# Kernel optimization log

Measured on AMD Instinct MI355X. Metric: run time of the kernel, lower is better.

The kernel has to match this reference:

```python
import jax, jax.numpy as jnp
import numpy as np

B, L, C, H, F = 1, 256, 256, 8, 512
D = C // H
SCALE = D ** -0.5
EPS = 1e-5


def _ln(x, g, b):
    m = jnp.mean(x, axis=-1, keepdims=True)
    v = jnp.mean((x - m) ** 2, axis=-1, keepdims=True)
    return (x - m) * jax.lax.rsqrt(v + EPS) * g + b


def setup_inputs() -> dict:
    key = jax.random.key(0)
    ks = jax.random.split(key, 16)
    w = lambda k, shp: jax.random.normal(k, shp, dtype=jnp.float32) * 0.02
    return {
        "pair_repr": jax.random.normal(ks[0], (B, L, L, C), dtype=jnp.float32),
        "pair_bias": jax.random.normal(ks[1], (B, H, L, L), dtype=jnp.float32),
        "Wq": w(ks[2], (C, C)), "bq": jnp.zeros((C,), jnp.float32),
        "Wk": w(ks[3], (C, C)), "bk": jnp.zeros((C,), jnp.float32),
        "Wv": w(ks[4], (C, C)), "bv": jnp.zeros((C,), jnp.float32),
        "Wo": w(ks[5], (C, C)), "bo": jnp.zeros((C,), jnp.float32),
        "W1": w(ks[6], (F, C)), "b1": jnp.zeros((F,), jnp.float32),
        "W2": w(ks[7], (C, F)), "b2": jnp.zeros((C,), jnp.float32),
        "g1": jnp.ones((C,), jnp.float32), "be1": jnp.zeros((C,), jnp.float32),
        "g2": jnp.ones((C,), jnp.float32), "be2": jnp.zeros((C,), jnp.float32),
        "mask": jnp.ones((B, L, L), dtype=jnp.int32),
    }


def reference(pair_repr, pair_bias, Wq, bq, Wk, bk, Wv, bv, Wo, bo,
              W1, b1, W2, b2, g1, be1, g2, be2, mask):
    x = _ln(pair_repr, g1, be1)
    # projections, split heads: [B, Li, Lj, H, D]
    q = (x @ Wq.T + bq).reshape(B, L, L, H, D)
    k = (x @ Wk.T + bk).reshape(B, L, L, H, D)
    v = (x @ Wv.T + bv).reshape(B, L, L, H, D)
    # attention per column j over rows: scores[b,j,h,i,i2]
    scores = jnp.einsum('bijhd,bkjhd->bjhik', q, k) * SCALE
    scores = scores + pair_bias[:, None]           # broadcast over j
    scores = jnp.where(mask[:, None, None, :, :] == 0, -jnp.inf, scores)
    probs = jax.nn.softmax(scores, axis=-1)
    attn = jnp.einsum('bjhik,bkjhd->bijhd', probs, v).reshape(B, L, L, C)
    attn = attn @ Wo.T + bo
    pr = pair_repr + attn                          # dropout is identity in eval
    y = _ln(pr, g2, be2)
    ff = jnp.maximum(y @ W1.T + b1, 0.0) @ W2.T + b2
    return pr + ff
```

## Files before the change

### kernel.cpp

```cpp
#include <hip/hip_runtime.h>

#define L_ 256
#define C_ 256
#define H_ 8
#define D_ 32
#define F_ 512
#define M_ (L_*L_)
#define SCALE2_ 0.2550348564624926f
#define LOG2E_  1.4426950408889634f

typedef __attribute__((ext_vector_type(8))) short v8s;
typedef __attribute__((ext_vector_type(4))) float v4f;
typedef __attribute__((ext_vector_type(16))) float v16f;
#define Z16 (v16f){0,0,0,0,0,0,0,0,0,0,0,0,0,0,0,0}

__device__ __forceinline__ ushort f2bf(float f) {
  union { float f; unsigned u; } v; v.f = f;
  unsigned r = v.u + 0x7FFFu + ((v.u >> 16) & 1u);
  return (ushort)(r >> 16);
}

__device__ __forceinline__ float bf2f(ushort u) {
  union { unsigned u; float f; } v; v.u = (unsigned)u << 16;
  return v.f;
}

__device__ __forceinline__ uint cvtpk(float lo, float hi) {
  uint r;
  asm("v_cvt_pk_bf16_f32 %0, %1, %2" : "=v"(r) : "v"(lo), "v"(hi));
  return r;
}

__device__ __forceinline__ void gload16(const void* g, void* l) {
  __builtin_amdgcn_global_load_lds(
      (const __attribute__((address_space(1))) void*)g,
      (__attribute__((address_space(3))) void*)l, 16, 0, 0);
}

__device__ __forceinline__ void pl32swap(uint &a, uint &b) {
  asm volatile("v_permlane32_swap_b32 %0, %1" : "+v"(a), "+v"(b));
}

__global__ __launch_bounds__(256) void prep_k(
    const float* __restrict__ Wq, const float* __restrict__ Wk,
    const float* __restrict__ Wv, const float* __restrict__ Wo,
    const float* __restrict__ W1, const float* __restrict__ W2,
    const float* __restrict__ bq, const float* __restrict__ bk,
    const float* __restrict__ bv,
    const float* __restrict__ bias, const int* __restrict__ mask,
    ushort* __restrict__ Wqkvb, ushort* __restrict__ Wob,
    ushort* __restrict__ W1b, ushort* __restrict__ W2b,
    float* __restrict__ bqkv, float* __restrict__ bM4) {
  int idx = blockIdx.x * 256 + threadIdx.x;
  if (idx < 49152) {
    int e = idx * 4; int n = e >> 8; int k = e & 255;
    const float* src = n < 256 ? &Wq[n*256 + k]
                     : n < 512 ? &Wk[(n-256)*256 + k]
                               : &Wv[(n-512)*256 + k];
    float4 f = *(const float4*)src;
    ushort4 o = { f2bf(f.x), f2bf(f.y), f2bf(f.z), f2bf(f.w) };
    *(ushort4*)&Wqkvb[e] = o;
  } else if (idx < 65536) {
    int e = (idx - 49152) * 4;
    float4 f = *(const float4*)&Wo[e];
    ushort4 o = { f2bf(f.x), f2bf(f.y), f2bf(f.z), f2bf(f.w) };
    *(ushort4*)&Wob[e] = o;
  } else if (idx < 98304) {
    int e = (idx - 65536) * 4;
    float4 f = *(const float4*)&W1[e];
    ushort4 o = { f2bf(f.x), f2bf(f.y), f2bf(f.z), f2bf(f.w) };
    *(ushort4*)&W1b[e] = o;
  } else if (idx < 131072) {
    int e = (idx - 98304) * 4;
    float4 f = *(const float4*)&W2[e];
    ushort4 o = { f2bf(f.x), f2bf(f.y), f2bf(f.z), f2bf(f.w) };
    *(ushort4*)&W2b[e] = o;
  } else if (idx < 262144) {
    int eb = idx - 131072;
    int q32 = eb & 31, r4 = (eb >> 5) & 3, h5 = (eb >> 7) & 1;
    int c = (eb >> 8) & 7, qb = (eb >> 11) & 7, h = eb >> 14;
    int q = qb*32 + q32;
    int keyb = 32*c + 8*r4 + 4*h5;
    float4 b4 = *(const float4*)&bias[((size_t)(h*256 + q))*256 + keyb];
    int4   m4 = *(const int4*)&mask[(size_t)q*256 + keyb];
    float4 o;
    o.x = m4.x ? b4.x * LOG2E_ - 8.0f : -1e30f;
    o.y = m4.y ? b4.y * LOG2E_ - 8.0f : -1e30f;
    o.z = m4.z ? b4.z * LOG2E_ - 8.0f : -1e30f;
    o.w = m4.w ? b4.w * LOG2E_ - 8.0f : -1e30f;
    *(float4*)&bM4[(size_t)eb*4] = o;
  } else if (idx < 262336) {
    int e = (idx - 262144) * 4;
    const float* src = e < 256 ? &bq[e] : e < 512 ? &bk[e-256] : &bv[e-512];
    *(float4*)&bqkv[e] = *(const float4*)src;
  }
}

template<bool TR>
__global__ __launch_bounds__(256) void ln_k(const float* __restrict__ in,
    const float* __restrict__ g, const float* __restrict__ b,
    ushort* __restrict__ out) {
  int wid = threadIdx.x >> 6, lane = threadIdx.x & 63;
  size_t row = (size_t)blockIdx.x * 4 + wid;
  const float* x = in + row * C_;
  float4 v = *(const float4*)&x[lane*4];
  float s  = v.x + v.y + v.z + v.w;
  float s2 = v.x*v.x + v.y*v.y + v.z*v.z + v.w*v.w;
  #pragma unroll
  for (int off = 1; off < 64; off <<= 1) {
    s  += __shfl_xor(s,  off);
    s2 += __shfl_xor(s2, off);
  }
  float mean = s * (1.0f/C_);
  float var  = s2 * (1.0f/C_) - mean*mean;
  float inv  = rsqrtf(var + 1e-5f);
  float4 gg = *(const float4*)&g[lane*4];
  float4 bb = *(const float4*)&b[lane*4];
  ushort4 o;
  o.x = f2bf((v.x-mean)*inv*gg.x + bb.x);
  o.y = f2bf((v.y-mean)*inv*gg.y + bb.y);
  o.z = f2bf((v.z-mean)*inv*gg.z + bb.z);
  o.w = f2bf((v.w-mean)*inv*gg.w + bb.w);
  size_t orow = TR ? ((row & 255) * 256 + (row >> 8)) : row;
  *(ushort4*)&out[orow*C_ + lane*4] = o;
}

template<bool OUTBF16, bool RELU, bool ADD, bool ADDB, bool QKV>
__global__ __launch_bounds__(256) void gemm5(
    const ushort* __restrict__ A, const ushort* __restrict__ W,
    const float* __restrict__ bias, const void* Rp,
    void* Optr, int N, int K, int lda, int ldo, int nby) {
  __shared__ __align__(16) ushort LDSb[2][128][64];
  constexpr bool LDST = QKV || (OUTBF16 && !ADD && !ADDB);
  int f = blockIdx.x;
  int sw = (f & 7) * (gridDim.x >> 3) + (f >> 3);
  const int bm = (sw / nby) * 128;
  const int bn = (sw % nby) * 128;
  const int t  = threadIdx.x;
  const int lane = t & 63, w = t >> 6;
  const int wm = (w >> 1) * 64, wn = (w & 1) * 64;
  const int lg = lane >> 4, lc = lane & 15;
  const int srow0 = t >> 3;
  const int scc   = t & 7;

  v4f acc[4][4];
  #pragma unroll
  for (int i = 0; i < 4; ++i)
    #pragma unroll
    for (int jj = 0; jj < 4; ++jj) acc[i][jj] = (v4f){0.f,0.f,0.f,0.f};

  for (int k0 = 0; k0 < K; k0 += 64) {
    #pragma unroll
    for (int s = 0; s < 4; ++s) {
      int row = s*32 + srow0;
      int gc  = (scc ^ (row & 7)) * 8;
      gload16(&A[(size_t)(bm + row)*lda + k0 + gc], (char*)LDSb + s*4096 + t*16);
      gload16(&W[(size_t)(bn + row)*K  + k0 + gc], (char*)LDSb + 16384 + s*4096 + t*16);
    }
    __syncthreads();
    #pragma unroll
    for (int kh = 0; kh < 2; ++kh) {
      v8s af[4], bf_[4];
      #pragma unroll
      for (int mi = 0; mi < 4; ++mi) {
        int row = wm + mi*16 + lc;
        int cd  = ((kh*4 + lg) ^ (row & 7)) * 16;
        af[mi] = *(const v8s*)((const char*)LDSb + row*128 + cd);
      }
      #pragma unroll
      for (int ni = 0; ni < 4; ++ni) {
        int row = wn + ni*16 + lc;
        int cd  = ((kh*4 + lg) ^ (row & 7)) * 16;
        bf_[ni] = *(const v8s*)((const char*)LDSb + 16384 + row*128 + cd);
      }
      #pragma unroll
      for (int mi = 0; mi < 4; ++mi)
        #pragma unroll
        for (int ni = 0; ni < 4; ++ni)
          acc[mi][ni] = __builtin_amdgcn_mfma_f32_16x16x32_bf16(bf_[ni], af[mi], acc[mi][ni], 0, 0, 0);
    }
    __syncthreads();
  }
  if (LDST) {
    ushort* T = (ushort*)LDSb;
    #pragma unroll
    for (int mi = 0; mi < 4; ++mi) {
      int row = wm + mi*16 + lc;
      #pragma unroll
      for (int ni = 0; ni < 4; ++ni) {
        int col = wn + ni*16 + lg*4;
        float4 bv = *(const float4*)&bias[bn + col];
        float o0 = acc[mi][ni][0] + bv.x;
        float o1 = acc[mi][ni][1] + bv.y;
        float o2 = acc[mi][ni][2] + bv.z;
        float o3 = acc[mi][ni][3] + bv.w;
        if (RELU) {
          o0 = fmaxf(o0, 0.f); o1 = fmaxf(o1, 0.f);
          o2 = fmaxf(o2, 0.f); o3 = fmaxf(o3, 0.f);
        }
        uint2 pw;
        pw.x = cvtpk(o0, o1);
        pw.y = cvtpk(o2, o3);
        *(uint2*)&T[row*128 + (col ^ ((row & 7) << 3))] = pw;
      }
    }
    __syncthreads();
    #pragma unroll
    for (int rr = 0; rr < 8; ++rr) {
      int row = rr*16 + (t >> 4);
      int cc  = t & 15;
      int sc  = cc ^ (row & 7);
      v8s vv = *(const v8s*)&T[row*128 + sc*8];
      if (QKV) {
        int m = bm + row;
        int jj = m >> 8, i = m & 255;
        int n = bn + cc*8;
        int c = n & 255, proj = n >> 8;
        int hh = c >> 5, dd = c & 31;
        size_t idx = (size_t)proj*16777216 + (((size_t)hh*256 + jj)*256 + i)*32 + dd;
        *(v8s*)&((ushort*)Optr)[idx] = vv;
      } else {
        *(v8s*)&((ushort*)Optr)[(size_t)(bm + row)*ldo + bn + cc*8] = vv;
      }
    }
  } else {
    #pragma unroll
    for (int mi = 0; mi < 4; ++mi) {
      int m = bm + wm + mi*16 + lc;
      #pragma unroll
      for (int ni = 0; ni < 4; ++ni) {
        int n0 = bn + wn + ni*16 + lg*4;
        float4 bv = *(const float4*)&bias[n0];
        float o0 = acc[mi][ni][0] + bv.x;
        float o1 = acc[mi][ni][1] + bv.y;
        float o2 = acc[mi][ni][2] + bv.z;
        float o3 = acc[mi][ni][3] + bv.w;
        if (RELU) {
          o0 = fmaxf(o0, 0.f); o1 = fmaxf(o1, 0.f);
          o2 = fmaxf(o2, 0.f); o3 = fmaxf(o3, 0.f);
        }
        size_t idx = (size_t)m * ldo + n0;
        if (ADD) {
          float4 r4 = *(const float4*)&((const float*)Rp)[idx];
          o0 += r4.x; o1 += r4.y; o2 += r4.z; o3 += r4.w;
        }
        if (ADDB) {
          uint2 rb = *(const uint2*)&((const ushort*)Rp)[idx];
          o0 += bf2f((ushort)(rb.x & 0xFFFF));
          o1 += bf2f((ushort)(rb.x >> 16));
          o2 += bf2f((ushort)(rb.y & 0xFFFF));
          o3 += bf2f((ushort)(rb.y >> 16));
        }
        if (OUTBF16) {
          uint2 pr;
          pr.x = cvtpk(o0, o1);
          pr.y = cvtpk(o2, o3);
          *(uint2*)&((ushort*)Optr)[idx] = pr;
        } else {
          float4 so = {o0, o1, o2, o3};
          *(float4*)&((float*)Optr)[idx] = so;
        }
      }
    }
  }
}

__global__ __launch_bounds__(512) void wo_ln_k(
    const ushort* A, const ushort* __restrict__ W,
    const float* __restrict__ bo, const float* __restrict__ R,
    ushort* prb,
    const float* __restrict__ g2, const float* __restrict__ be2,
    ushort* __restrict__ yb) {
  __shared__ __align__(16) ushort As[128][64];
  __shared__ __align__(16) ushort Bs[256][64];
  int f = blockIdx.x;
  int sw = (f & 7) * (gridDim.x >> 3) + (f >> 3);
  const int bm = sw * 128;
  const int t  = threadIdx.x;
  const int lane = t & 63, w = t >> 6;
  const int wm = (w >> 2) * 64, wn = (w & 3) * 64;
  const int lg = lane >> 4, lc = lane & 15;
  const int srow0 = t >> 3;
  const int scc   = t & 7;

  v4f acc[4][4];
  #pragma unroll
  for (int i = 0; i < 4; ++i)
    #pragma unroll
    for (int jj = 0; jj < 4; ++jj) acc[i][jj] = (v4f){0.f,0.f,0.f,0.f};

  for (int k0 = 0; k0 < 256; k0 += 64) {
    #pragma unroll
    for (int s = 0; s < 2; ++s) {
      int row = s*64 + srow0;
      int gc  = (scc ^ (row & 7)) * 8;
      gload16(&A[(size_t)(bm + row)*256 + k0 + gc], (char*)As + s*8192 + t*16);
    }
    #pragma unroll
    for (int s = 0; s < 4; ++s) {
      int row = s*64 + srow0;
      int gc  = (scc ^ (row & 7)) * 8;
      gload16(&W[(size_t)row*256 + k0 + gc], (char*)Bs + s*8192 + t*16);
    }
    __syncthreads();
    #pragma unroll
    for (int kh = 0; kh < 2; ++kh) {
      v8s af[4], bf_[4];
      #pragma unroll
      for (int mi = 0; mi < 4; ++mi) {
        int row = wm + mi*16 + lc;
        int cd  = ((kh*4 + lg) ^ (row & 7)) * 16;
        af[mi] = *(const v8s*)((const char*)As + row*128 + cd);
      }
      #pragma unroll
      for (int ni = 0; ni < 4; ++ni) {
        int row = wn + ni*16 + lc;
        int cd  = ((kh*4 + lg) ^ (row & 7)) * 16;
        bf_[ni] = *(const v8s*)((const char*)Bs + row*128 + cd);
      }
      #pragma unroll
      for (int mi = 0; mi < 4; ++mi)
        #pragma unroll
        for (int ni = 0; ni < 4; ++ni)
          acc[mi][ni] = __builtin_amdgcn_mfma_f32_16x16x32_bf16(bf_[ni], af[mi], acc[mi][ni], 0, 0, 0);
    }
    __syncthreads();
  }

  float sum_mi[4], ssq_mi[4];
  #pragma unroll
  for (int mi = 0; mi < 4; ++mi) {
    int m = bm + wm + mi*16 + lc;
    float sm = 0.f, sq = 0.f;
    #pragma unroll
    for (int ni = 0; ni < 4; ++ni) {
      int n0 = wn + ni*16 + lg*4;
      float4 bv = *(const float4*)&bo[n0];
      float4 r4 = *(const float4*)&R[(size_t)m*256 + n0];
      float p0 = acc[mi][ni][0] + bv.x + r4.x;
      float p1 = acc[mi][ni][1] + bv.y + r4.y;
      float p2 = acc[mi][ni][2] + bv.z + r4.z;
      float p3 = acc[mi][ni][3] + bv.w + r4.w;
      acc[mi][ni][0] = p0; acc[mi][ni][1] = p1;
      acc[mi][ni][2] = p2; acc[mi][ni][3] = p3;
      uint2 pw;
      pw.x = cvtpk(p0, p1);
      pw.y = cvtpk(p2, p3);
      *(uint2*)&prb[(size_t)m*256 + n0] = pw;
      sm += (p0 + p1) + (p2 + p3);
      sq += (p0*p0 + p1*p1) + (p2*p2 + p3*p3);
    }
    sum_mi[mi] = sm; ssq_mi[mi] = sq;
  }
  #pragma unroll
  for (int mi = 0; mi < 4; ++mi) {
    sum_mi[mi] += __shfl_xor(sum_mi[mi], 16);
    sum_mi[mi] += __shfl_xor(sum_mi[mi], 32);
    ssq_mi[mi] += __shfl_xor(ssq_mi[mi], 16);
    ssq_mi[mi] += __shfl_xor(ssq_mi[mi], 32);
  }
  float* sbuf = (float*)As;
  if (lg == 0) {
    #pragma unroll
    for (int mi = 0; mi < 4; ++mi) {
      int idx = w*64 + mi*16 + lc;
      sbuf[idx]       = sum_mi[mi];
      sbuf[512 + idx] = ssq_mi[mi];
    }
  }
  __syncthreads();
  #pragma unroll
  for (int mi = 0; mi < 4; ++mi) {
    int bi = (w >> 2)*256 + mi*16 + lc;
    float s = (sbuf[bi] + sbuf[bi+64]) + (sbuf[bi+128] + sbuf[bi+192]);
    float q = (sbuf[512+bi] + sbuf[512+bi+64]) + (sbuf[512+bi+128] + sbuf[512+bi+192]);
    float mu  = s * (1.0f/256.0f);
    float inv = rsqrtf(q * (1.0f/256.0f) - mu*mu + 1e-5f);
    int m = bm + wm + mi*16 + lc;
    #pragma unroll
    for (int ni = 0; ni < 4; ++ni) {
      int n0 = wn + ni*16 + lg*4;
      float4 gg = *(const float4*)&g2[n0];
      float4 bb = *(const float4*)&be2[n0];
      float y0 = (acc[mi][ni][0] - mu)*inv*gg.x + bb.x;
      float y1 = (acc[mi][ni][1] - mu)*inv*gg.y + bb.y;
      float y2 = (acc[mi][ni][2] - mu)*inv*gg.z + bb.z;
      float y3 = (acc[mi][ni][3] - mu)*inv*gg.w + bb.w;
      uint2 pr;
      pr.x = cvtpk(y0, y1);
      pr.y = cvtpk(y2, y3);
      *(uint2*)&yb[(size_t)m*256 + n0] = pr;
    }
  }
}

__global__ __launch_bounds__(256, 4) void attn10(
    const ushort* __restrict__ qt, const ushort* __restrict__ kt,
    const ushort* __restrict__ vt, const float* __restrict__ bM4,
    ushort* __restrict__ ao) {
  __shared__ __align__(16) ushort Vt[32][264];
  __shared__ __align__(16) ushort Ks[256][36];
  const int j = blockIdx.x & 255, h = blockIdx.x >> 8;
  const int t = threadIdx.x, w = t >> 6, lane = t & 63;
  const int l5 = lane & 31, h5 = lane >> 5;
  const size_t base = ((size_t)(h*256 + j)) * 8192;

  {
    const ushort* vsrc = vt + base;
    int k4 = (t & 63) * 4, sd = (t >> 6) * 8;
    v8s v0 = *(const v8s*)&vsrc[(k4+0)*32 + sd];
    v8s v1 = *(const v8s*)&vsrc[(k4+1)*32 + sd];
    v8s v2 = *(const v8s*)&vsrc[(k4+2)*32 + sd];
    v8s v3 = *(const v8s*)&vsrc[(k4+3)*32 + sd];
    #pragma unroll
    for (int u = 0; u < 8; ++u) {
      ushort4 q4 = { (ushort)v0[u], (ushort)v1[u], (ushort)v2[u], (ushort)v3[u] };
      *(ushort4*)&Vt[sd+u][k4] = q4;
    }
    const ushort* ksrcg = kt + base;
    #pragma unroll
    for (int s = 0; s < 4; ++s) {
      int el = s*2048 + t*8;
      v8s kv = *(const v8s*)&ksrcg[el];
      *(v8s*)&Ks[el >> 5][el & 31] = kv;
    }
  }
  __syncthreads();

  const ushort* qsrc = qt + base;

  #pragma unroll 1
  for (int qi = 0; qi < 2; ++qi) {
    const int qb = w*2 + qi;
    v8s qf0 = *(const v8s*)&qsrc[(qb*32 + l5)*32 + h5*8];
    v8s qf1 = *(const v8s*)&qsrc[(qb*32 + l5)*32 + 16 + h5*8];
    const float* bqb = bM4 + (size_t)(h*8 + qb) * 8192;
    v16f o = Z16;
    float l = 0.f;

    #pragma unroll 2
    for (int c = 0; c < 8; ++c) {
      v8s kf0 = *(const v8s*)&Ks[c*32 + l5][h5*8];
      v8s kf1 = *(const v8s*)&Ks[c*32 + l5][16 + h5*8];
      v16f s = __builtin_amdgcn_mfma_f32_32x32x16_bf16(kf0, qf0, Z16, 0, 0, 0);
      s = __builtin_amdgcn_mfma_f32_32x32x16_bf16(kf1, qf1, s, 0, 0, 0);
      float p[16];
      #pragma unroll
      for (int r4 = 0; r4 < 4; ++r4) {
        float4 b4 = *(const float4*)&bqb[((c*2 + h5)*4 + r4)*128 + l5*4];
        p[r4*4+0] = __builtin_amdgcn_exp2f(fmaf(s[r4*4+0], SCALE2_, b4.x));
        p[r4*4+1] = __builtin_amdgcn_exp2f(fmaf(s[r4*4+1], SCALE2_, b4.y));
        p[r4*4+2] = __builtin_amdgcn_exp2f(fmaf(s[r4*4+2], SCALE2_, b4.z));
        p[r4*4+3] = __builtin_amdgcn_exp2f(fmaf(s[r4*4+3], SCALE2_, b4.w));
      }
      #pragma unroll
      for (int r = 0; r < 16; ++r) l += p[r];
      uint pk[8];
      #pragma unroll
      for (int i2 = 0; i2 < 8; ++i2)
        pk[i2] = cvtpk(p[2*i2], p[2*i2+1]);
      uint w0 = pk[0], w2 = pk[2]; pl32swap(w0, w2);
      uint w1 = pk[1], w3 = pk[3]; pl32swap(w1, w3);
      uint w4 = pk[4], w6 = pk[6]; pl32swap(w4, w6);
      uint w5 = pk[5], w7 = pk[7]; pl32swap(w5, w7);
      uint4 B1 = {w0, w1, w2, w3};
      uint4 B2 = {w4, w5, w6, w7};
      v8s vv1 = *(const v8s*)&Vt[l5][c*32 + h5*8];
      v8s vv2 = *(const v8s*)&Vt[l5][c*32 + 16 + h5*8];
      o = __builtin_amdgcn_mfma_f32_32x32x16_bf16(vv1, *(v8s*)&B1, o, 0, 0, 0);
      o = __builtin_amdgcn_mfma_f32_32x32x16_bf16(vv2, *(v8s*)&B2, o, 0, 0, 0);
    }
    float lt = l + __shfl_xor(l, 32);
    float inv = 1.0f / lt;
    size_t ob = ((size_t)(qb*32 + l5)*256 + j)*256 + h*32;
    #pragma unroll
    for (int r4 = 0; r4 < 4; ++r4) {
      uint2 pr;
      pr.x = cvtpk(o[4*r4+0]*inv, o[4*r4+1]*inv);
      pr.y = cvtpk(o[4*r4+2]*inv, o[4*r4+3]*inv);
      *(uint2*)&ao[ob + 8*r4 + 4*h5] = pr;
    }
  }
}

extern "C" void kernel_launch(void* const* d_in, const int* in_sizes, int n_in,
                              void* d_out, int out_size, void* d_ws, size_t ws_size,
                              hipStream_t stream) {
  const float* pair_repr = (const float*)d_in[0];
  const float* pair_bias = (const float*)d_in[1];
  const float* Wq = (const float*)d_in[2];
  const float* bq = (const float*)d_in[3];
  const float* Wk = (const float*)d_in[4];
  const float* bk = (const float*)d_in[5];
  const float* Wv = (const float*)d_in[6];
  const float* bv = (const float*)d_in[7];
  const float* Wo = (const float*)d_in[8];
  const float* bo = (const float*)d_in[9];
  const float* W1 = (const float*)d_in[10];
  const float* b1 = (const float*)d_in[11];
  const float* W2 = (const float*)d_in[12];
  const float* b2 = (const float*)d_in[13];
  const float* g1 = (const float*)d_in[14];
  const float* be1= (const float*)d_in[15];
  const float* g2 = (const float*)d_in[16];
  const float* be2= (const float*)d_in[17];
  const int* mask = (const int*)d_in[18];
  float* out = (float*)d_out;

  char* wsb = (char*)d_ws;
  ushort* xb = (ushort*)wsb;
  ushort* ao = (ushort*)wsb;
  ushort* prb = (ushort*)wsb;
  ushort* qt = (ushort*)(wsb + 33554432);
  ushort* yb = qt;
  ushort* kt = (ushort*)(wsb + 67108864);
  ushort* vt = (ushort*)(wsb + 100663296);
  ushort* hb = kt;
  char* d0 = wsb + 134217728;
  ushort* Wqkvb = (ushort*)d0;
  ushort* Wob   = (ushort*)(d0 + 393216);
  ushort* W1b   = (ushort*)(d0 + 524288);
  ushort* W2b   = (ushort*)(d0 + 786432);
  float*  bqkv  = (float*)(d0 + 1048576);
  float*  bM4   = (float*)(d0 + 1052672);

  prep_k<<<dim3(1025), 256, 0, stream>>>(Wq, Wk, Wv, Wo, W1, W2, bq, bk, bv,
                                         pair_bias, mask, Wqkvb, Wob, W1b, W2b, bqkv, bM4);
  ln_k<true><<<dim3(M_/4), 256, 0, stream>>>(pair_repr, g1, be1, xb);
  gemm5<true,false,false,false,true><<<dim3(3072), 256, 0, stream>>>(
      xb, Wqkvb, bqkv, nullptr, (void*)qt, 768, C_, C_, 0, 6);
  attn10<<<dim3(L_*H_), 256, 0, stream>>>(qt, kt, vt, bM4, ao);
  wo_ln_k<<<dim3(512), 512, 0, stream>>>(ao, Wob, bo, pair_repr, prb, g2, be2, yb);
  gemm5<true,true,false,false,false><<<dim3(2048), 256, 0, stream>>>(
      yb, W1b, b1, nullptr, (void*)hb, F_, C_, C_, F_, 4);
  gemm5<false,false,false,true,false><<<dim3(1024), 256, 0, stream>>>(
      hb, W2b, b2, prb, out, C_, F_, F_, C_, 2);
}
```

Measured before the change: 214.1 us.

## Widen GEMM block tile to 128x256 with 512 threads

Replaces the 128x128 tile, 256-thread GEMM with a 128x256 tile run by 8 waves, so each loaded A tile is reused across twice as many output columns and half as many blocks are launched. The LDS-staged epilogue now writes the output in two 128-column halves with extra barriers, so the transpose buffer fits in the shared memory. The unused fp32 residual-add path is removed. The cost is more LDS per block and fewer blocks, which may lower occupancy and leave the grid less evenly spread across CUs.

Measured after the change: 199.3 us, median of 2. -6.9%, faster.

```diff
diff --git a/kernel.cpp b/kernel.cpp
--- a/kernel.cpp
+++ b/kernel.cpp
@@ -125,20 +125,20 @@
   *(ushort4*)&out[orow*C_ + lane*4] = o;
 }
 
-template<bool OUTBF16, bool RELU, bool ADD, bool ADDB, bool QKV>
-__global__ __launch_bounds__(256) void gemm5(
+template<bool OUTBF16, bool RELU, bool ADDB, bool QKV>
+__global__ __launch_bounds__(512) void gemm6(
     const ushort* __restrict__ A, const ushort* __restrict__ W,
     const float* __restrict__ bias, const void* Rp,
     void* Optr, int N, int K, int lda, int ldo, int nby) {
-  __shared__ __align__(16) ushort LDSb[2][128][64];
-  constexpr bool LDST = QKV || (OUTBF16 && !ADD && !ADDB);
+  __shared__ __align__(16) ushort LDSb[384][64];
+  constexpr bool LDST = QKV || (OUTBF16 && !ADDB);
   int f = blockIdx.x;
   int sw = (f & 7) * (gridDim.x >> 3) + (f >> 3);
   const int bm = (sw / nby) * 128;
-  const int bn = (sw % nby) * 128;
+  const int bn = (sw % nby) * 256;
   const int t  = threadIdx.x;
   const int lane = t & 63, w = t >> 6;
-  const int wm = (w >> 1) * 64, wn = (w & 1) * 64;
+  const int wm = (w >> 2) * 64, wn = (w & 3) * 64;
   const int lg = lane >> 4, lc = lane & 15;
   const int srow0 = t >> 3;
   const int scc   = t & 7;
@@ -151,11 +151,16 @@
 
   for (int k0 = 0; k0 < K; k0 += 64) {
     #pragma unroll
+    for (int s = 0; s < 2; ++s) {
+      int row = s*64 + srow0;
+      int gc  = (scc ^ (row & 7)) * 8;
+      gload16(&A[(size_t)(bm + row)*lda + k0 + gc], (char*)LDSb + s*8192 + t*16);
+    }
+    #pragma unroll
     for (int s = 0; s < 4; ++s) {
-      int row = s*32 + srow0;
+      int row = s*64 + srow0;
       int gc  = (scc ^ (row & 7)) * 8;
-      gload16(&A[(size_t)(bm + row)*lda + k0 + gc], (char*)LDSb + s*4096 + t*16);
-      gload16(&W[(size_t)(bn + row)*K  + k0 + gc], (char*)LDSb + 16384 + s*4096 + t*16);
+      gload16(&W[(size_t)(bn + row)*K + k0 + gc], (char*)LDSb + 16384 + s*8192 + t*16);
     }
     __syncthreads();
     #pragma unroll
@@ -184,44 +189,50 @@
   if (LDST) {
     ushort* T = (ushort*)LDSb;
     #pragma unroll
-    for (int mi = 0; mi < 4; ++mi) {
-      int row = wm + mi*16 + lc;
-      #pragma unroll
-      for (int ni = 0; ni < 4; ++ni) {
-        int col = wn + ni*16 + lg*4;
-        float4 bv = *(const float4*)&bias[bn + col];
-        float o0 = acc[mi][ni][0] + bv.x;
-        float o1 = acc[mi][ni][1] + bv.y;
-        float o2 = acc[mi][ni][2] + bv.z;
-        float o3 = acc[mi][ni][3] + bv.w;
-        if (RELU) {
-          o0 = fmaxf(o0, 0.f); o1 = fmaxf(o1, 0.f);
-          o2 = fmaxf(o2, 0.f); o3 = fmaxf(o3, 0.f);
+    for (int nh = 0; nh < 2; ++nh) {
+      if (((w & 3) >> 1) == nh) {
+        #pragma unroll
+        for (int mi = 0; mi < 4; ++mi) {
+          int row = wm + mi*16 + lc;
+          #pragma unroll
+          for (int ni = 0; ni < 4; ++ni) {
+            int col = wn + ni*16 + lg*4;
+            float4 bv = *(const float4*)&bias[bn + col];
+            float o0 = acc[mi][ni][0] + bv.x;
+            float o1 = acc[mi][ni][1] + bv.y;
+            float o2 = acc[mi][ni][2] + bv.z;
+            float o3 = acc[mi][ni][3] + bv.w;
+            if (RELU) {
+              o0 = fmaxf(o0, 0.f); o1 = fmaxf(o1, 0.f);
+              o2 = fmaxf(o2, 0.f); o3 = fmaxf(o3, 0.f);
+            }
+            uint2 pw;
+            pw.x = cvtpk(o0, o1);
+            pw.y = cvtpk(o2, o3);
+            *(uint2*)&T[row*128 + ((col & 127) ^ ((row & 7) << 3))] = pw;
+          }
         }
-        uint2 pw;
-        pw.x = cvtpk(o0, o1);
-        pw.y = cvtpk(o2, o3);
-        *(uint2*)&T[row*128 + (col ^ ((row & 7) << 3))] = pw;
-      }
-    }
-    __syncthreads();
-    #pragma unroll
-    for (int rr = 0; rr < 8; ++rr) {
-      int row = rr*16 + (t >> 4);
-      int cc  = t & 15;
-      int sc  = cc ^ (row & 7);
-      v8s vv = *(const v8s*)&T[row*128 + sc*8];
-      if (QKV) {
-        int m = bm + row;
-        int jj = m >> 8, i = m & 255;
-        int n = bn + cc*8;
-        int c = n & 255, proj = n >> 8;
-        int hh = c >> 5, dd = c & 31;
-        size_t idx = (size_t)proj*16777216 + (((size_t)hh*256 + jj)*256 + i)*32 + dd;
-        *(v8s*)&((ushort*)Optr)[idx] = vv;
-      } else {
-        *(v8s*)&((ushort*)Optr)[(size_t)(bm + row)*ldo + bn + cc*8] = vv;
-      }
+      }
+      __syncthreads();
+      #pragma unroll
+      for (int rr = 0; rr < 4; ++rr) {
+        int row = rr*32 + (t >> 4);
+        int cc  = t & 15;
+        int sc  = cc ^ (row & 7);
+        v8s vv = *(const v8s*)&T[row*128 + sc*8];
+        if (QKV) {
+          int m = bm + row;
+          int jj = m >> 8, i = m & 255;
+          int n = bn + nh*128 + cc*8;
+          int c = n & 255, proj = n >> 8;
+          int hh = c >> 5, dd = c & 31;
+          size_t idx = (size_t)proj*16777216 + (((size_t)hh*256 + jj)*256 + i)*32 + dd;
+          *(v8s*)&((ushort*)Optr)[idx] = vv;
+        } else {
+          *(v8s*)&((ushort*)Optr)[(size_t)(bm + row)*ldo + bn + nh*128 + cc*8] = vv;
+        }
+      }
+      __syncthreads();
     }
   } else {
     #pragma unroll
@@ -240,10 +251,6 @@
           o2 = fmaxf(o2, 0.f); o3 = fmaxf(o3, 0.f);
         }
         size_t idx = (size_t)m * ldo + n0;
-        if (ADD) {
-          float4 r4 = *(const float4*)&((const float*)Rp)[idx];
-          o0 += r4.x; o1 += r4.y; o2 += r4.z; o3 += r4.w;
-        }
         if (ADDB) {
           uint2 rb = *(const uint2*)&((const ushort*)Rp)[idx];
           o0 += bf2f((ushort)(rb.x & 0xFFFF));
@@ -527,12 +534,12 @@
   prep_k<<<dim3(1025), 256, 0, stream>>>(Wq, Wk, Wv, Wo, W1, W2, bq, bk, bv,
                                          pair_bias, mask, Wqkvb, Wob, W1b, W2b, bqkv, bM4);
   ln_k<true><<<dim3(M_/4), 256, 0, stream>>>(pair_repr, g1, be1, xb);
-  gemm5<true,false,false,false,true><<<dim3(3072), 256, 0, stream>>>(
-      xb, Wqkvb, bqkv, nullptr, (void*)qt, 768, C_, C_, 0, 6);
+  gemm6<true,false,false,true><<<dim3(1536), 512, 0, stream>>>(
+      xb, Wqkvb, bqkv, nullptr, (void*)qt, 768, C_, C_, 0, 3);
   attn10<<<dim3(L_*H_), 256, 0, stream>>>(qt, kt, vt, bM4, ao);
   wo_ln_k<<<dim3(512), 512, 0, stream>>>(ao, Wob, bo, pair_repr, prb, g2, be2, yb);
-  gemm5<true,true,false,false,false><<<dim3(2048), 256, 0, stream>>>(
-      yb, W1b, b1, nullptr, (void*)hb, F_, C_, C_, F_, 4);
-  gemm5<false,false,false,true,false><<<dim3(1024), 256, 0, stream>>>(
-      hb, W2b, b2, prb, out, C_, F_, F_, C_, 2);
-}
+  gemm6<true,true,false,false><<<dim3(1024), 512, 0, stream>>>(
+      yb, W1b, b1, nullptr, (void*)hb, F_, C_, C_, F_, 2);
+  gemm6<false,false,true,false><<<dim3(512), 512, 0, stream>>>(
+      hb, W2b, b2, prb, out, C_, F_, F_, C_, 1);
+}
```
